# Kernel tuning notes

Hardware: AMD Instinct MI355X
Metric: run time of the kernel (lower is better)

## Reference

```python
import jax, jax.numpy as jnp
import numpy as np

B, C, H, W = 8, 256, 64, 64
D = C // 8  # qk proj dim = 32
R = C // 8  # channel-SE reduction dim = 32

def setup_inputs() -> dict:
    key = jax.random.key(0)
    ks = jax.random.split(key, 10)
    s = lambda *sh: 1.0 / np.sqrt(sh[-1])
    return {
        'x':  jax.random.normal(ks[0], (B, C, H, W), jnp.float32),
        'Wq': jax.random.normal(ks[1], (D, C), jnp.float32) * s(D, C),
        'bq': jnp.zeros((D,), jnp.float32),
        'Wk': jax.random.normal(ks[2], (D, C), jnp.float32) * s(D, C),
        'bk': jnp.zeros((D,), jnp.float32),
        'Wv': jax.random.normal(ks[3], (C, C), jnp.float32) * s(C, C),
        'bv': jnp.zeros((C,), jnp.float32),
        'gamma': jnp.ones((1,), jnp.float32),
        'W1': jax.random.normal(ks[4], (R, 2 * C), jnp.float32) * s(R, 2 * C),
        'W2': jax.random.normal(ks[5], (C, R), jnp.float32) * s(C, R),
        'lamb': jnp.ones((1,), jnp.float32),
    }

def reference(x, Wq, bq, Wk, bk, Wv, bv, gamma, W1, W2, lamb):
    b, c, h, w = x.shape
    n = h * w
    xf = x.reshape(b, c, n)  # [B,C,N]
    # --- spatial self-attention (1x1 convs == matmuls over channel dim) ---
    q = jnp.einsum('dc,bcn->bnd', Wq, xf) + bq            # [B,N,D]
    k = jnp.einsum('dc,bcn->bdn', Wk, xf) + bk[:, None]   # [B,D,N]
    attn = jax.nn.softmax(jnp.einsum('bnd,bdm->bnm', q, k), axis=-1)  # [B,N,N]
    v = jnp.einsum('dc,bcn->bdn', Wv, xf) + bv[:, None]   # [B,C,N]
    # out[b,c,m] = sum_n v[b,c,n] * attn[b,m,n]  (torch: bmm(v, attn^T))
    sp = jnp.einsum('bcn,bmn->bcm', v, attn).reshape(b, c, h, w)
    sp = gamma * sp
    # --- channel SE-gate ---
    mean = jnp.mean(xf, axis=-1)                # [B,C]
    std = jnp.std(xf, axis=-1, ddof=1)          # torch.std uses unbiased (ddof=1)
    inp = jnp.concatenate([mean, std], axis=1)  # [B,2C]
    a = jax.nn.sigmoid(jax.nn.relu(inp @ W1.T) @ W2.T)  # [B,C]
    ch = lamb * a[:, :, None, None] * x
    return sp + ch + x
```

## Files before the change

### kernel.cpp

```cpp
#include <hip/hip_runtime.h>
#include <hip/hip_bf16.h>

#define Bb 8
#define Cc 256
#define Nn 4096
#define Dd 32

typedef short bf16x8 __attribute__((ext_vector_type(8)));
typedef short bf16x4 __attribute__((ext_vector_type(4)));
typedef float f32x4 __attribute__((ext_vector_type(4)));
typedef unsigned int u32;

__device__ __forceinline__ void glds16(const void* g, void* l) {
    __builtin_amdgcn_global_load_lds(
        (const __attribute__((address_space(1))) unsigned int*)g,
        (__attribute__((address_space(3))) unsigned int*)l, 16, 0, 0);
}

__device__ __forceinline__ u32 pkbf16(float a, float b) {
    return ((u32)__bfloat16_as_ushort(__float2bfloat16(b)) << 16) |
           (u32)__bfloat16_as_ushort(__float2bfloat16(a));
}

__global__ __launch_bounds__(256) void wconv_kernel(
    const float* __restrict__ Wq, const float* __restrict__ Wk, const float* __restrict__ Wv,
    __hip_bfloat16* __restrict__ w_bf, float* __restrict__ stats )
{
    const int ct = blockIdx.x;
    const int t = threadIdx.x;
    for (int k = ct * 256 + t; k < 2 * Bb * Cc; k += 5 * 256) stats[k] = 0.f;
#pragma unroll
    for (int i = 0; i < 8; i++) {
        int g = i * 256 + t;
        int row = g >> 5, c8 = g & 31;
        int c0 = c8 * 8;
        int grow = ct * 64 + row;
        const float* src;
        if (grow < 32)       src = Wq + (size_t)grow * Cc + c0;
        else if (grow < 64)  src = Wk + (size_t)(grow - 32) * Cc + c0;
        else                 src = Wv + (size_t)(grow - 64) * Cc + c0;
        float4 v0 = *(const float4*)src;
        float4 v1 = *(const float4*)(src + 4);
        bf16x8 o;
        o[0] = __bfloat16_as_short(__float2bfloat16(v0.x));
        o[1] = __bfloat16_as_short(__float2bfloat16(v0.y));
        o[2] = __bfloat16_as_short(__float2bfloat16(v0.z));
        o[3] = __bfloat16_as_short(__float2bfloat16(v0.w));
        o[4] = __bfloat16_as_short(__float2bfloat16(v1.x));
        o[5] = __bfloat16_as_short(__float2bfloat16(v1.y));
        o[6] = __bfloat16_as_short(__float2bfloat16(v1.z));
        o[7] = __bfloat16_as_short(__float2bfloat16(v1.w));
        int kchunk = c0 >> 5, qd = (c0 & 31) >> 3, cg = row >> 4, rl = row & 15;
        *(bf16x8*)(w_bf + ((size_t)ct * 32 + kchunk * 4 + cg) * 512 + (qd * 16 + rl) * 8) = o;
    }
}

__global__ __launch_bounds__(256, 2) void proj_kernel(
    const float* __restrict__ x, const __hip_bfloat16* __restrict__ w_bf,
    const float* __restrict__ bq, const float* __restrict__ bk, const float* __restrict__ bv,
    __hip_bfloat16* __restrict__ q_ws, __hip_bfloat16* __restrict__ k_ws,
    __hip_bfloat16* __restrict__ v_ws,
    float* __restrict__ sum_ws, float* __restrict__ sumsq_ws)
{
    __shared__ __hip_bfloat16 tile[64][68];
    __shared__ __hip_bfloat16 ldsX[32 * 512];
    __shared__ __hip_bfloat16 ldsW[32 * 512];

    const int n0 = blockIdx.x * 64;
    const int b  = blockIdx.y;
    const int t = threadIdx.x;
    const int w = t >> 6, lane = t & 63, quad = lane >> 4, l15 = lane & 15;

    float4 xv[4][4];
#pragma unroll
    for (int cq = 0; cq < 4; cq++)
#pragma unroll
        for (int i = 0; i < 4; i++) {
            int id = i * 256 + t;
            int row = id >> 4, col4 = id & 15;
            xv[cq][i] = *(const float4*)(x + ((size_t)(b * Cc + cq * 64 + row)) * Nn + n0 + col4 * 4);
        }

#pragma unroll
    for (int j = 0; j < 8; j++) {
        int idx = w * 8 + j;
        glds16(w_bf + (size_t)idx * 512 + lane * 8, ldsW + idx * 512);
    }

#pragma unroll
    for (int cq = 0; cq < 4; cq++) {
#pragma unroll
        for (int i = 0; i < 4; i++) {
            int id = i * 256 + t;
            int row = id >> 4, col4 = id & 15;
            float4 v = xv[cq][i];
            bf16x4 bv4;
            bv4[0] = __bfloat16_as_short(__float2bfloat16(v.x));
            bv4[1] = __bfloat16_as_short(__float2bfloat16(v.y));
            bv4[2] = __bfloat16_as_short(__float2bfloat16(v.z));
            bv4[3] = __bfloat16_as_short(__float2bfloat16(v.w));
            *(bf16x4*)((void*)&tile[row][col4 * 4]) = bv4;
            float ls  = v.x + v.y + v.z + v.w;
            float ls2 = v.x * v.x + v.y * v.y + v.z * v.z + v.w * v.w;
            ls  += __shfl_xor(ls, 1, 16);  ls2 += __shfl_xor(ls2, 1, 16);
            ls  += __shfl_xor(ls, 2, 16);  ls2 += __shfl_xor(ls2, 2, 16);
            ls  += __shfl_xor(ls, 4, 16);  ls2 += __shfl_xor(ls2, 4, 16);
            ls  += __shfl_xor(ls, 8, 16);  ls2 += __shfl_xor(ls2, 8, 16);
            if ((t & 15) == 0) {
                atomicAdd(&sum_ws[b * Cc + cq * 64 + row], ls);
                atomicAdd(&sumsq_ws[b * Cc + cq * 64 + row], ls2);
            }
        }
        __syncthreads();
#pragma unroll
        for (int it = 0; it < 2; it++) {
            int id = it * 256 + t;
            int nl = id >> 3, cg = id & 7;
            bf16x8 o;
#pragma unroll
            for (int j = 0; j < 8; j++) o[j] = __bfloat16_as_short(tile[cg * 8 + j][nl]);
            int kchunk = cq * 2 + (cg >> 2);
            int cquad  = cg & 3;
            int ngrp = nl >> 4, nlo = nl & 15;
            *(bf16x8*)(ldsX + ((size_t)(kchunk * 4 + ngrp) * 512) + (cquad * 16 + nlo) * 8) = o;
        }
        __syncthreads();
    }

    for (int ct = 0; ct < 5; ct++) {
        f32x4 acc[4];
#pragma unroll
        for (int cg = 0; cg < 4; cg++) {
            int gcol = ct * 64 + cg * 16 + l15;
            float bias = (gcol < 32) ? bq[gcol] : (gcol < 64 ? bk[gcol - 32] : bv[gcol - 64]);
            acc[cg] = (f32x4){bias, bias, bias, bias};
        }

#pragma unroll
        for (int kchunk = 0; kchunk < 8; kchunk++) {
            bf16x8 a = *(const bf16x8*)(ldsX + ((kchunk * 4 + w) * 64 + lane) * 8);
#pragma unroll
            for (int cg = 0; cg < 4; cg++) {
                bf16x8 bw = *(const bf16x8*)(ldsW + ((kchunk * 4 + cg) * 64 + lane) * 8);
                acc[cg] = __builtin_amdgcn_mfma_f32_16x16x32_bf16(a, bw, acc[cg], 0, 0, 0);
            }
        }

#pragma unroll
        for (int cg = 0; cg < 4; cg++) {
            int gcol = ct * 64 + cg * 16 + l15;
            int nb = n0 + w * 16 + quad * 4;
            if (gcol < 64) {
                __hip_bfloat16* dst = (gcol < 32) ? q_ws : k_ws;
                int d = gcol & 31;
#pragma unroll
                for (int r = 0; r < 4; r++)
                    dst[((size_t)(b * Nn + nb + r)) * Dd + d] = __float2bfloat16(acc[cg][r]);
            } else {
                int c = gcol - 64;
                bf16x4 o;
#pragma unroll
                for (int r = 0; r < 4; r++) o[r] = __bfloat16_as_short(__float2bfloat16(acc[cg][r]));
                *(bf16x4*)(v_ws + ((size_t)(b * Cc + c)) * Nn + nb) = o;
            }
        }

        if (ct < 4) {
            __syncthreads();
#pragma unroll
            for (int j = 0; j < 8; j++) {
                int idx = w * 8 + j;
                glds16(w_bf + ((size_t)(ct + 1) * 32 + idx) * 512 + lane * 8, ldsW + idx * 512);
            }
            __syncthreads();
        }
    }
}

__global__ __launch_bounds__(256) void gate_kernel(
    const float* __restrict__ sum_ws, const float* __restrict__ sumsq_ws,
    const float* __restrict__ W1, const float* __restrict__ W2,
    const float* __restrict__ lamb, float* __restrict__ coef)
{
    int b = blockIdx.x;
    __shared__ float inp[2 * Cc];
    __shared__ float h[32];
    int t = threadIdx.x;
    float s  = sum_ws[b * Cc + t];
    float s2 = sumsq_ws[b * Cc + t];
    float m   = s / Nn;
    float var = (s2 - (float)Nn * m * m) / (float)(Nn - 1);
    inp[t]      = m;
    inp[Cc + t] = sqrtf(fmaxf(var, 0.f));
    __syncthreads();
    if (t < 32) {
        float a = 0.f;
        for (int i = 0; i < 2 * Cc; i++) a += W1[t * (2 * Cc) + i] * inp[i];
        h[t] = fmaxf(a, 0.f);
    }
    __syncthreads();
    float g = 0.f;
#pragma unroll
    for (int r = 0; r < 32; r++) g += W2[t * 32 + r] * h[r];
    float a = 1.f / (1.f + __expf(-g));
    coef[b * Cc + t] = 1.f + lamb[0] * a;
}

__global__ __launch_bounds__(512, 2) void attn_kernel(
    const __hip_bfloat16* __restrict__ q_ws, const __hip_bfloat16* __restrict__ k_ws,
    const __hip_bfloat16* __restrict__ v_ws, const float* __restrict__ coef,
    const float* __restrict__ x, const float* __restrict__ gamma_p,
    float* __restrict__ out)
{
    extern __shared__ __hip_bfloat16 smem[];
    __hip_bfloat16 *vcur = smem, *vnext = smem + 16384, *vnn = smem + 32768;
    __hip_bfloat16 *kA = smem + 49152, *kB = smem + 53248, *kC = smem + 57344;

    const int b  = blockIdx.x & 7;
    const int m0 = (blockIdx.x >> 3) * 128;
    const int t = threadIdx.x;
    const int w = t >> 6, lane = t & 63, quad = lane >> 4, l15 = lane & 15;
    const int p = w >> 2, pw = w & 3;

    const bf16x8 aq0 = *(const bf16x8*)(q_ws + ((size_t)(b * Nn + m0 + (2 * pw)     * 16 + l15)) * Dd + quad * 8);
    const bf16x8 aq1 = *(const bf16x8*)(q_ws + ((size_t)(b * Nn + m0 + (2 * pw + 1) * 16 + l15)) * Dd + quad * 8);

    const __hip_bfloat16* vsrc[4];
#pragma unroll
    for (int j = 0; j < 4; j++) {
        int idx = w * 4 + j;
        int ch = idx >> 4, tc = idx & 15;
        vsrc[j] = v_ws + ((size_t)(b * Cc + tc * 16 + l15)) * Nn + ch * 32 + quad * 8;
    }
    const int sl15 = (l15 & 3) | ((l15 & 4) << 1) | ((l15 & 8) >> 1);
    const __hip_bfloat16* ksrc = k_ws + ((size_t)(b * Nn + w * 16 + sl15)) * Dd + quad * 8;

#pragma unroll
    for (int j = 0; j < 4; j++) glds16(vsrc[j], vcur + (w * 4 + j) * 512);
#pragma unroll
    for (int j = 0; j < 4; j++) glds16(vsrc[j] + 64, vnext + (w * 4 + j) * 512);
    glds16(ksrc, kA + w * 512);
    glds16(ksrc + (size_t)128 * Dd, kB + w * 512);
    __syncthreads();

    f32x4 acc[2][16];
#pragma unroll
    for (int i = 0; i < 2; i++)
#pragma unroll
        for (int j = 0; j < 16; j++) acc[i][j] = (f32x4){0.f, 0.f, 0.f, 0.f};
    float lsum0 = 0.f, lsum1 = 0.f;

    const int NIT = Nn / 64;

    u32 pc0[2][2], pc1[2][2];
#pragma unroll
    for (int j = 0; j < 2; j++) {
        bf16x8 ak = *(const bf16x8*)(kA + ((2 * p + j) * 64 + lane) * 8);
        f32x4 s0 = __builtin_amdgcn_mfma_f32_16x16x32_bf16(ak, aq0, (f32x4){0.f,0.f,0.f,0.f}, 0, 0, 0);
        f32x4 s1 = __builtin_amdgcn_mfma_f32_16x16x32_bf16(ak, aq1, (f32x4){0.f,0.f,0.f,0.f}, 0, 0, 0);
        float a0 = __expf(s0[0]), a1 = __expf(s0[1]), a2 = __expf(s0[2]), a3 = __expf(s0[3]);
        lsum0 += (a0 + a1) + (a2 + a3);
        pc0[j][0] = pkbf16(a0, a1); pc0[j][1] = pkbf16(a2, a3);
        float b0 = __expf(s1[0]), b1 = __expf(s1[1]), b2 = __expf(s1[2]), b3 = __expf(s1[3]);
        lsum1 += (b0 + b1) + (b2 + b3);
        pc1[j][0] = pkbf16(b0, b1); pc1[j][1] = pkbf16(b2, b3);
    }

    for (int it = 0; it < NIT; it++) {
        if (it + 2 < NIT) {
#pragma unroll
            for (int j = 0; j < 4; j++)
                glds16(vsrc[j] + (size_t)(it + 2) * 64, vnn + (w * 4 + j) * 512);
        }
        if ((it & 1) == 0 && (it >> 1) + 2 < 32)
            glds16(ksrc + (size_t)(((it >> 1) + 2) * 128) * Dd, kC + w * 512);

        auto g0 = __builtin_amdgcn_permlane32_swap(pc0[0][0], pc0[1][0], false, false);
        auto g1 = __builtin_amdgcn_permlane32_swap(pc0[0][1], pc0[1][1], false, false);
        auto h0 = __builtin_amdgcn_permlane32_swap(pc1[0][0], pc1[1][0], false, false);
        auto h1 = __builtin_amdgcn_permlane32_swap(pc1[0][1], pc1[1][1], false, false);
        union { u32 uw[4]; bf16x8 v; } bp0, bp1;
        bp0.uw[0] = g0[0]; bp0.uw[1] = g1[0]; bp0.uw[2] = g0[1]; bp0.uw[3] = g1[1];
        bp1.uw[0] = h0[0]; bp1.uw[1] = h1[0]; bp1.uw[2] = h0[1]; bp1.uw[3] = h1[1];

        u32 pn0[2][2], pn1[2][2];
        const int itn = (it + 1 < NIT) ? it + 1 : NIT - 1;
        const __hip_bfloat16* kb = (((itn >> 1) > (it >> 1)) ? kB : kA) + (itn & 1) * 2048;
        float nls0 = 0.f, nls1 = 0.f;
#pragma unroll
        for (int j = 0; j < 2; j++) {
            bf16x8 ak = *(const bf16x8*)(kb + ((2 * p + j) * 64 + lane) * 8);
            f32x4 s0 = __builtin_amdgcn_mfma_f32_16x16x32_bf16(ak, aq0, (f32x4){0.f,0.f,0.f,0.f}, 0, 0, 0);
            f32x4 s1 = __builtin_amdgcn_mfma_f32_16x16x32_bf16(ak, aq1, (f32x4){0.f,0.f,0.f,0.f}, 0, 0, 0);
            float a0 = __expf(s0[0]), a1 = __expf(s0[1]), a2 = __expf(s0[2]), a3 = __expf(s0[3]);
            nls0 += (a0 + a1) + (a2 + a3);
            pn0[j][0] = pkbf16(a0, a1); pn0[j][1] = pkbf16(a2, a3);
            float b0 = __expf(s1[0]), b1 = __expf(s1[1]), b2 = __expf(s1[2]), b3 = __expf(s1[3]);
            nls1 += (b0 + b1) + (b2 + b3);
            pn1[j][0] = pkbf16(b0, b1); pn1[j][1] = pkbf16(b2, b3);
        }
        if (it + 1 < NIT) { lsum0 += nls0; lsum1 += nls1; }

#pragma unroll
        for (int cf = 0; cf < 16; cf++) {
            bf16x8 av = *(const bf16x8*)(vcur + ((p * 16 + cf) * 64 + lane) * 8);
            acc[0][cf] = __builtin_amdgcn_mfma_f32_16x16x32_bf16(av, bp0.v, acc[0][cf], 0, 0, 0);
            acc[1][cf] = __builtin_amdgcn_mfma_f32_16x16x32_bf16(av, bp1.v, acc[1][cf], 0, 0, 0);
        }

#pragma unroll
        for (int j = 0; j < 2; j++)
#pragma unroll
            for (int k = 0; k < 2; k++) { pc0[j][k] = pn0[j][k]; pc1[j][k] = pn1[j][k]; }

        { __hip_bfloat16* vt = vcur; vcur = vnext; vnext = vnn; vnn = vt; }
        if (it & 1) { __hip_bfloat16* kt = kA; kA = kB; kB = kC; kC = kt; }

        if (it + 2 < NIT)
            asm volatile("s_waitcnt vmcnt(4)\n\ts_barrier" ::: "memory");
        else
            asm volatile("s_waitcnt vmcnt(0)\n\ts_barrier" ::: "memory");
    }

    float* lex = (float*)(smem + 32768);
    lex[w * 128 + lane]      = lsum0;
    lex[w * 128 + 64 + lane] = lsum1;
    f32x4* exv = (f32x4*)smem;
#pragma unroll
    for (int mfi = 0; mfi < 2; mfi++) {
        __syncthreads();
        if (p == 0) {
#pragma unroll
            for (int j = 0; j < 8; j++) exv[(w * 8 + j) * 64 + lane] = acc[mfi][8 + j];
        } else {
#pragma unroll
            for (int j = 0; j < 8; j++) exv[(w * 8 + j) * 64 + lane] = acc[mfi][j];
        }
        __syncthreads();
        if (p == 0) {
#pragma unroll
            for (int j = 0; j < 8; j++) acc[mfi][j] += exv[((w ^ 4) * 8 + j) * 64 + lane];
        } else {
#pragma unroll
            for (int j = 0; j < 8; j++) acc[mfi][8 + j] += exv[((w ^ 4) * 8 + j) * 64 + lane];
        }
        if (mfi == 0) {
            lsum0 += lex[(w ^ 4) * 128 + lane];
            lsum1 += lex[(w ^ 4) * 128 + 64 + lane];
        }
    }

    lsum0 += __shfl_xor(lsum0, 16); lsum0 += __shfl_xor(lsum0, 32);
    lsum1 += __shfl_xor(lsum1, 16); lsum1 += __shfl_xor(lsum1, 32);
    const float g = gamma_p[0];
    const float inv0 = g / lsum0, inv1 = g / lsum1;

    if (p == 0) {
#pragma unroll
        for (int j = 0; j < 8; j++) {
#pragma unroll
            for (int r = 0; r < 4; r++) {
                int c = j * 16 + quad * 4 + r;
                float cfv = coef[b * Cc + c];
                size_t base = ((size_t)(b * Cc + c)) * Nn + m0 + (2 * pw) * 16 + l15;
                out[base]      = acc[0][j][r] * inv0 + cfv * x[base];
                out[base + 16] = acc[1][j][r] * inv1 + cfv * x[base + 16];
            }
        }
    } else {
#pragma unroll
        for (int j = 0; j < 8; j++) {
#pragma unroll
            for (int r = 0; r < 4; r++) {
                int c = (8 + j) * 16 + quad * 4 + r;
                float cfv = coef[b * Cc + c];
                size_t base = ((size_t)(b * Cc + c)) * Nn + m0 + (2 * pw) * 16 + l15;
                out[base]      = acc[0][8 + j][r] * inv0 + cfv * x[base];
                out[base + 16] = acc[1][8 + j][r] * inv1 + cfv * x[base + 16];
            }
        }
    }
}

extern "C" void kernel_launch(void* const* d_in, const int* in_sizes, int n_in,
                              void* d_out, int out_size, void* d_ws, size_t ws_size,
                              hipStream_t stream) {
    const float* x     = (const float*)d_in[0];
    const float* Wq    = (const float*)d_in[1];
    const float* bq    = (const float*)d_in[2];
    const float* Wk    = (const float*)d_in[3];
    const float* bk    = (const float*)d_in[4];
    const float* Wv    = (const float*)d_in[5];
    const float* bv    = (const float*)d_in[6];
    const float* gamma = (const float*)d_in[7];
    const float* W1    = (const float*)d_in[8];
    const float* W2    = (const float*)d_in[9];
    const float* lamb  = (const float*)d_in[10];
    float* out = (float*)d_out;

    char* ws = (char*)d_ws;
    __hip_bfloat16* q_ws = (__hip_bfloat16*)ws;
    __hip_bfloat16* k_ws = (__hip_bfloat16*)(ws + (2u  << 20));
    __hip_bfloat16* v_ws = (__hip_bfloat16*)(ws + (4u  << 20));
    float* sum_ws   = (float*)(ws + (36u << 20));
    float* sumsq_ws = sum_ws + Bb * Cc;
    float* coef     = sumsq_ws + Bb * Cc;
    __hip_bfloat16* w_bf = (__hip_bfloat16*)(ws + (37u << 20));

    (void)hipFuncSetAttribute((const void*)attn_kernel,
                              hipFuncAttributeMaxDynamicSharedMemorySize, 122880);

    wconv_kernel<<<5, 256, 0, stream>>>(Wq, Wk, Wv, w_bf, sum_ws);
    proj_kernel<<<dim3(Nn / 64, Bb), 256, 0, stream>>>(x, w_bf, bq, bk, bv,
                                                       q_ws, k_ws, v_ws, sum_ws, sumsq_ws);
    gate_kernel<<<Bb, 256, 0, stream>>>(sum_ws, sumsq_ws, W1, W2, lamb, coef);
    attn_kernel<<<256, 512, 122880, stream>>>(q_ws, k_ws, v_ws, coef, x, gamma, out);
}
```

Measured before the change: 227.5 us.

## Halve attention query tile to 64 rows and double-buffer for higher occupancy

The attention kernel now processes 64 query rows per block instead of 128, which doubles the grid to 512 blocks. It drops from triple to double buffering of V and K in LDS, cutting shared memory from 120KB to 80KB, and raises the launch-bounds minimum to 4 blocks. The aim is to fit more blocks and waves per CU to hide latency. In exchange, each V/K tile loaded from L2 and LDS now feeds half as many MFMAs, global V traffic doubles, and the fine-grained vmcnt wait is replaced by a full __syncthreads with less prefetch depth. The tighter register budget from the new launch bounds may also cause spills.

After: 276.1 us. 1.21x slower.

```diff
diff --git a/kernel.cpp b/kernel.cpp
--- a/kernel.cpp
+++ b/kernel.cpp
@@ -206,24 +206,25 @@
     coef[b * Cc + t] = 1.f + lamb[0] * a;
 }
 
-__global__ __launch_bounds__(512, 2) void attn_kernel(
+__global__ __launch_bounds__(512, 4) void attn_kernel(
     const __hip_bfloat16* __restrict__ q_ws, const __hip_bfloat16* __restrict__ k_ws,
     const __hip_bfloat16* __restrict__ v_ws, const float* __restrict__ coef,
     const float* __restrict__ x, const float* __restrict__ gamma_p,
     float* __restrict__ out)
 {
     extern __shared__ __hip_bfloat16 smem[];
-    __hip_bfloat16 *vcur = smem, *vnext = smem + 16384, *vnn = smem + 32768;
-    __hip_bfloat16 *kA = smem + 49152, *kB = smem + 53248, *kC = smem + 57344;
+    __hip_bfloat16* vbuf0 = smem;
+    __hip_bfloat16* vbuf1 = smem + 16384;
+    __hip_bfloat16* kbuf0 = smem + 32768;
+    __hip_bfloat16* kbuf1 = smem + 36864;
 
     const int b  = blockIdx.x & 7;
-    const int m0 = (blockIdx.x >> 3) * 128;
+    const int m0 = (blockIdx.x >> 3) * 64;
     const int t = threadIdx.x;
     const int w = t >> 6, lane = t & 63, quad = lane >> 4, l15 = lane & 15;
     const int p = w >> 2, pw = w & 3;
 
-    const bf16x8 aq0 = *(const bf16x8*)(q_ws + ((size_t)(b * Nn + m0 + (2 * pw)     * 16 + l15)) * Dd + quad * 8);
-    const bf16x8 aq1 = *(const bf16x8*)(q_ws + ((size_t)(b * Nn + m0 + (2 * pw + 1) * 16 + l15)) * Dd + quad * 8);
+    const bf16x8 aq = *(const bf16x8*)(q_ws + ((size_t)(b * Nn + m0 + pw * 16 + l15)) * Dd + quad * 8);
 
     const __hip_bfloat16* vsrc[4];
 #pragma unroll
@@ -236,124 +237,96 @@
     const __hip_bfloat16* ksrc = k_ws + ((size_t)(b * Nn + w * 16 + sl15)) * Dd + quad * 8;
 
 #pragma unroll
-    for (int j = 0; j < 4; j++) glds16(vsrc[j], vcur + (w * 4 + j) * 512);
-#pragma unroll
-    for (int j = 0; j < 4; j++) glds16(vsrc[j] + 64, vnext + (w * 4 + j) * 512);
-    glds16(ksrc, kA + w * 512);
-    glds16(ksrc + (size_t)128 * Dd, kB + w * 512);
+    for (int j = 0; j < 4; j++) glds16(vsrc[j], vbuf0 + (w * 4 + j) * 512);
+    glds16(ksrc, kbuf0 + w * 512);
     __syncthreads();
 
-    f32x4 acc[2][16];
-#pragma unroll
-    for (int i = 0; i < 2; i++)
-#pragma unroll
-        for (int j = 0; j < 16; j++) acc[i][j] = (f32x4){0.f, 0.f, 0.f, 0.f};
-    float lsum0 = 0.f, lsum1 = 0.f;
+    f32x4 acc[16];
+#pragma unroll
+    for (int j = 0; j < 16; j++) acc[j] = (f32x4){0.f, 0.f, 0.f, 0.f};
+    float lsum = 0.f;
 
     const int NIT = Nn / 64;
 
-    u32 pc0[2][2], pc1[2][2];
+    u32 pc[2][2];
 #pragma unroll
     for (int j = 0; j < 2; j++) {
-        bf16x8 ak = *(const bf16x8*)(kA + ((2 * p + j) * 64 + lane) * 8);
-        f32x4 s0 = __builtin_amdgcn_mfma_f32_16x16x32_bf16(ak, aq0, (f32x4){0.f,0.f,0.f,0.f}, 0, 0, 0);
-        f32x4 s1 = __builtin_amdgcn_mfma_f32_16x16x32_bf16(ak, aq1, (f32x4){0.f,0.f,0.f,0.f}, 0, 0, 0);
-        float a0 = __expf(s0[0]), a1 = __expf(s0[1]), a2 = __expf(s0[2]), a3 = __expf(s0[3]);
-        lsum0 += (a0 + a1) + (a2 + a3);
-        pc0[j][0] = pkbf16(a0, a1); pc0[j][1] = pkbf16(a2, a3);
-        float b0 = __expf(s1[0]), b1 = __expf(s1[1]), b2 = __expf(s1[2]), b3 = __expf(s1[3]);
-        lsum1 += (b0 + b1) + (b2 + b3);
-        pc1[j][0] = pkbf16(b0, b1); pc1[j][1] = pkbf16(b2, b3);
+        bf16x8 ak = *(const bf16x8*)(kbuf0 + ((2 * p + j) * 64 + lane) * 8);
+        f32x4 s = __builtin_amdgcn_mfma_f32_16x16x32_bf16(ak, aq, (f32x4){0.f,0.f,0.f,0.f}, 0, 0, 0);
+        float a0 = __expf(s[0]), a1 = __expf(s[1]), a2 = __expf(s[2]), a3 = __expf(s[3]);
+        lsum += (a0 + a1) + (a2 + a3);
+        pc[j][0] = pkbf16(a0, a1); pc[j][1] = pkbf16(a2, a3);
     }
 
     for (int it = 0; it < NIT; it++) {
-        if (it + 2 < NIT) {
+        if (it + 1 < NIT) {
+            __hip_bfloat16* vn = ((it + 1) & 1) ? vbuf1 : vbuf0;
 #pragma unroll
             for (int j = 0; j < 4; j++)
-                glds16(vsrc[j] + (size_t)(it + 2) * 64, vnn + (w * 4 + j) * 512);
-        }
-        if ((it & 1) == 0 && (it >> 1) + 2 < 32)
-            glds16(ksrc + (size_t)(((it >> 1) + 2) * 128) * Dd, kC + w * 512);
-
-        auto g0 = __builtin_amdgcn_permlane32_swap(pc0[0][0], pc0[1][0], false, false);
-        auto g1 = __builtin_amdgcn_permlane32_swap(pc0[0][1], pc0[1][1], false, false);
-        auto h0 = __builtin_amdgcn_permlane32_swap(pc1[0][0], pc1[1][0], false, false);
-        auto h1 = __builtin_amdgcn_permlane32_swap(pc1[0][1], pc1[1][1], false, false);
-        union { u32 uw[4]; bf16x8 v; } bp0, bp1;
-        bp0.uw[0] = g0[0]; bp0.uw[1] = g1[0]; bp0.uw[2] = g0[1]; bp0.uw[3] = g1[1];
-        bp1.uw[0] = h0[0]; bp1.uw[1] = h1[0]; bp1.uw[2] = h0[1]; bp1.uw[3] = h1[1];
-
-        u32 pn0[2][2], pn1[2][2];
-        const int itn = (it + 1 < NIT) ? it + 1 : NIT - 1;
-        const __hip_bfloat16* kb = (((itn >> 1) > (it >> 1)) ? kB : kA) + (itn & 1) * 2048;
-        float nls0 = 0.f, nls1 = 0.f;
+                glds16(vsrc[j] + (size_t)(it + 1) * 64, vn + (w * 4 + j) * 512);
+        }
+        if ((it & 1) == 0 && it + 2 < NIT) {
+            int sl = (it >> 1) + 1;
+            glds16(ksrc + (size_t)(sl * 128) * Dd, ((sl & 1) ? kbuf1 : kbuf0) + w * 512);
+        }
+
+        auto g0 = __builtin_amdgcn_permlane32_swap(pc[0][0], pc[1][0], false, false);
+        auto g1 = __builtin_amdgcn_permlane32_swap(pc[0][1], pc[1][1], false, false);
+        union { u32 uw[4]; bf16x8 v; } bp;
+        bp.uw[0] = g0[0]; bp.uw[1] = g1[0]; bp.uw[2] = g0[1]; bp.uw[3] = g1[1];
+
+        u32 pn[2][2];
+        const int itn = (it + 1 < NIT) ? it + 1 : it;
+        const __hip_bfloat16* kbn = (((itn >> 1) & 1) ? kbuf1 : kbuf0) + (itn & 1) * 2048;
+        float nls = 0.f;
 #pragma unroll
         for (int j = 0; j < 2; j++) {
-            bf16x8 ak = *(const bf16x8*)(kb + ((2 * p + j) * 64 + lane) * 8);
-            f32x4 s0 = __builtin_amdgcn_mfma_f32_16x16x32_bf16(ak, aq0, (f32x4){0.f,0.f,0.f,0.f}, 0, 0, 0);
-            f32x4 s1 = __builtin_amdgcn_mfma_f32_16x16x32_bf16(ak, aq1, (f32x4){0.f,0.f,0.f,0.f}, 0, 0, 0);
-            float a0 = __expf(s0[0]), a1 = __expf(s0[1]), a2 = __expf(s0[2]), a3 = __expf(s0[3]);
-            nls0 += (a0 + a1) + (a2 + a3);
-            pn0[j][0] = pkbf16(a0, a1); pn0[j][1] = pkbf16(a2, a3);
-            float b0 = __expf(s1[0]), b1 = __expf(s1[1]), b2 = __expf(s1[2]), b3 = __expf(s1[3]);
-            nls1 += (b0 + b1) + (b2 + b3);
-            pn1[j][0] = pkbf16(b0, b1); pn1[j][1] = pkbf16(b2, b3);
-        }
-        if (it + 1 < NIT) { lsum0 += nls0; lsum1 += nls1; }
-
+            bf16x8 ak = *(const bf16x8*)(kbn + ((2 * p + j) * 64 + lane) * 8);
+            f32x4 s = __builtin_amdgcn_mfma_f32_16x16x32_bf16(ak, aq, (f32x4){0.f,0.f,0.f,0.f}, 0, 0, 0);
+            float a0 = __expf(s[0]), a1 = __expf(s[1]), a2 = __expf(s[2]), a3 = __expf(s[3]);
+            nls += (a0 + a1) + (a2 + a3);
+            pn[j][0] = pkbf16(a0, a1); pn[j][1] = pkbf16(a2, a3);
+        }
+        if (it + 1 < NIT) lsum += nls;
+
+        const __hip_bfloat16* vb = (it & 1) ? vbuf1 : vbuf0;
 #pragma unroll
         for (int cf = 0; cf < 16; cf++) {
-            bf16x8 av = *(const bf16x8*)(vcur + ((p * 16 + cf) * 64 + lane) * 8);
-            acc[0][cf] = __builtin_amdgcn_mfma_f32_16x16x32_bf16(av, bp0.v, acc[0][cf], 0, 0, 0);
-            acc[1][cf] = __builtin_amdgcn_mfma_f32_16x16x32_bf16(av, bp1.v, acc[1][cf], 0, 0, 0);
+            bf16x8 av = *(const bf16x8*)(vb + ((p * 16 + cf) * 64 + lane) * 8);
+            acc[cf] = __builtin_amdgcn_mfma_f32_16x16x32_bf16(av, bp.v, acc[cf], 0, 0, 0);
         }
 
 #pragma unroll
         for (int j = 0; j < 2; j++)
 #pragma unroll
-            for (int k = 0; k < 2; k++) { pc0[j][k] = pn0[j][k]; pc1[j][k] = pn1[j][k]; }
-
-        { __hip_bfloat16* vt = vcur; vcur = vnext; vnext = vnn; vnn = vt; }
-        if (it & 1) { __hip_bfloat16* kt = kA; kA = kB; kB = kC; kC = kt; }
-
-        if (it + 2 < NIT)
-            asm volatile("s_waitcnt vmcnt(4)\n\ts_barrier" ::: "memory");
-        else
-            asm volatile("s_waitcnt vmcnt(0)\n\ts_barrier" ::: "memory");
+            for (int k = 0; k < 2; k++) pc[j][k] = pn[j][k];
+
+        __syncthreads();
     }
 
     float* lex = (float*)(smem + 32768);
-    lex[w * 128 + lane]      = lsum0;
-    lex[w * 128 + 64 + lane] = lsum1;
     f32x4* exv = (f32x4*)smem;
-#pragma unroll
-    for (int mfi = 0; mfi < 2; mfi++) {
-        __syncthreads();
-        if (p == 0) {
-#pragma unroll
-            for (int j = 0; j < 8; j++) exv[(w * 8 + j) * 64 + lane] = acc[mfi][8 + j];
-        } else {
-#pragma unroll
-            for (int j = 0; j < 8; j++) exv[(w * 8 + j) * 64 + lane] = acc[mfi][j];
-        }
-        __syncthreads();
-        if (p == 0) {
-#pragma unroll
-            for (int j = 0; j < 8; j++) acc[mfi][j] += exv[((w ^ 4) * 8 + j) * 64 + lane];
-        } else {
-#pragma unroll
-            for (int j = 0; j < 8; j++) acc[mfi][8 + j] += exv[((w ^ 4) * 8 + j) * 64 + lane];
-        }
-        if (mfi == 0) {
-            lsum0 += lex[(w ^ 4) * 128 + lane];
-            lsum1 += lex[(w ^ 4) * 128 + 64 + lane];
-        }
-    }
-
-    lsum0 += __shfl_xor(lsum0, 16); lsum0 += __shfl_xor(lsum0, 32);
-    lsum1 += __shfl_xor(lsum1, 16); lsum1 += __shfl_xor(lsum1, 32);
+    lex[w * 64 + lane] = lsum;
+    if (p == 0) {
+#pragma unroll
+        for (int j = 0; j < 8; j++) exv[(w * 8 + j) * 64 + lane] = acc[8 + j];
+    } else {
+#pragma unroll
+        for (int j = 0; j < 8; j++) exv[(w * 8 + j) * 64 + lane] = acc[j];
+    }
+    __syncthreads();
+    if (p == 0) {
+#pragma unroll
+        for (int j = 0; j < 8; j++) acc[j] += exv[((w ^ 4) * 8 + j) * 64 + lane];
+    } else {
+#pragma unroll
+        for (int j = 0; j < 8; j++) acc[8 + j] += exv[((w ^ 4) * 8 + j) * 64 + lane];
+    }
+    lsum += lex[(w ^ 4) * 64 + lane];
+
+    lsum += __shfl_xor(lsum, 16); lsum += __shfl_xor(lsum, 32);
     const float g = gamma_p[0];
-    const float inv0 = g / lsum0, inv1 = g / lsum1;
+    const float inv = g / lsum;
 
     if (p == 0) {
 #pragma unroll
@@ -362,9 +335,8 @@
             for (int r = 0; r < 4; r++) {
                 int c = j * 16 + quad * 4 + r;
                 float cfv = coef[b * Cc + c];
-                size_t base = ((size_t)(b * Cc + c)) * Nn + m0 + (2 * pw) * 16 + l15;
-                out[base]      = acc[0][j][r] * inv0 + cfv * x[base];
-                out[base + 16] = acc[1][j][r] * inv1 + cfv * x[base + 16];
+                size_t base = ((size_t)(b * Cc + c)) * Nn + m0 + pw * 16 + l15;
+                out[base] = acc[j][r] * inv + cfv * x[base];
             }
         }
     } else {
@@ -374,9 +346,8 @@
             for (int r = 0; r < 4; r++) {
                 int c = (8 + j) * 16 + quad * 4 + r;
                 float cfv = coef[b * Cc + c];
-                size_t base = ((size_t)(b * Cc + c)) * Nn + m0 + (2 * pw) * 16 + l15;
-                out[base]      = acc[0][8 + j][r] * inv0 + cfv * x[base];
-                out[base + 16] = acc[1][8 + j][r] * inv1 + cfv * x[base + 16];
+                size_t base = ((size_t)(b * Cc + c)) * Nn + m0 + pw * 16 + l15;
+                out[base] = acc[8 + j][r] * inv + cfv * x[base];
             }
         }
     }
@@ -408,11 +379,11 @@
     __hip_bfloat16* w_bf = (__hip_bfloat16*)(ws + (37u << 20));
 
     (void)hipFuncSetAttribute((const void*)attn_kernel,
-                              hipFuncAttributeMaxDynamicSharedMemorySize, 122880);
+                              hipFuncAttributeMaxDynamicSharedMemorySize, 81920);
 
     wconv_kernel<<<5, 256, 0, stream>>>(Wq, Wk, Wv, w_bf, sum_ws);
     proj_kernel<<<dim3(Nn / 64, Bb), 256, 0, stream>>>(x, w_bf, bq, bk, bv,
                                                        q_ws, k_ws, v_ws, sum_ws, sumsq_ws);
     gate_kernel<<<Bb, 256, 0, stream>>>(sum_ws, sumsq_ws, W1, W2, lamb, coef);
-    attn_kernel<<<256, 512, 122880, stream>>>(q_ws, k_ws, v_ws, coef, x, gamma, out);
-}
+    attn_kernel<<<512, 512, 81920, stream>>>(q_ws, k_ws, v_ws, coef, x, gamma, out);
+}
```
